# Optimization experiments

Hardware: AMD Instinct MI355X
Metric: run time of the kernel (lower is better)

## Reference

```python
import jax, jax.numpy as jnp
import numpy as np

N, T, D = 50000, 16, 4          # nodes, timesteps, input features
E = 800000                      # edges
H, HID = 4, 32                  # GAT heads, hidden dim (concat=False -> mean over heads)
TH, THID = 4, 64                # temporal heads, temporal hidden (= 2*HID)
HD = THID // TH                 # temporal head dim
NEG_SLOPE = 0.2


def setup_inputs() -> dict:
    key = jax.random.key(0)
    ks = iter(jax.random.split(key, 64))
    nrm = lambda shape, s=0.05: jax.random.normal(next(ks), shape, dtype=jnp.float32) * s
    inp = {}
    inp["x"] = jax.random.normal(next(ks), (N, T, D), dtype=jnp.float32)
    inp["edge_index"] = jax.random.randint(next(ks), (2, E), 0, N)
    inp["edge_weight"] = jax.random.uniform(next(ks), (E,), dtype=jnp.float32)
    # input projection
    inp["in_W"], inp["in_b"] = nrm((D, HID)), nrm((HID,))
    # two GATv2 layers (lin_l, lin_r, lin_edge (no bias), att, out bias)
    for i in range(2):
        inp[f"g{i}_Wl"], inp[f"g{i}_bl"] = nrm((HID, H * HID)), nrm((H * HID,))
        inp[f"g{i}_Wr"], inp[f"g{i}_br"] = nrm((HID, H * HID)), nrm((H * HID,))
        inp[f"g{i}_We"] = nrm((1, H * HID))
        inp[f"g{i}_att"] = nrm((H, HID))
        inp[f"g{i}_bias"] = nrm((HID,))
    # temporal attention block
    inp["Wq"], inp["bq"] = nrm((HID, THID)), nrm((THID,))
    inp["Wk"], inp["bk"] = nrm((HID, THID)), nrm((THID,))
    inp["Wv"], inp["bv"] = nrm((HID, THID)), nrm((THID,))
    inp["Wo"], inp["bo"] = nrm((THID, HID)), nrm((HID,))
    # heads
    inp["fW1"], inp["fb1"] = nrm((HID, 32)), nrm((32,))
    inp["fW2"], inp["fb2"] = nrm((32, 1)), nrm((1,))
    inp["rW1"], inp["rb1"] = nrm((HID, 32)), nrm((32,))
    inp["rW2"], inp["rb2"] = nrm((32, 1)), nrm((1,))
    return inp


def _gatv2(xp, edge_index, edge_attr, Wl, bl, Wr, br, We, att, bias):
    """GATv2Conv, heads=H, concat=False (mean), edge_dim=1, no self loops."""
    src, dst = edge_index[0], edge_index[1]          # message src -> dst
    xl = (xp @ Wl + bl).reshape(N, H, HID)
    xr = (xp @ Wr + br).reshape(N, H, HID)
    ee = (edge_attr @ We).reshape(E, H, HID)
    m = xl[src] + xr[dst] + ee                       # (E,H,C)
    m = jnp.where(m > 0, m, NEG_SLOPE * m)           # leaky_relu
    logits = jnp.einsum('ehc,hc->eh', m, att)        # (E,H)
    mx = jax.ops.segment_max(logits, dst, num_segments=N)
    mx = jnp.where(jnp.isfinite(mx), mx, 0.0)
    a = jnp.exp(logits - mx[dst])
    denom = jax.ops.segment_sum(a, dst, num_segments=N)
    alpha = a / (denom[dst] + 1e-16)                 # segment softmax over dst
    out = jax.ops.segment_sum(alpha[:, :, None] * xl[src], dst, num_segments=N)
    return out.mean(axis=1) + bias                   # (N,HID)


def reference(x, edge_index, edge_weight,
              in_W, in_b,
              g0_Wl, g0_bl, g0_Wr, g0_br, g0_We, g0_att, g0_bias,
              g1_Wl, g1_bl, g1_Wr, g1_br, g1_We, g1_att, g1_bias,
              Wq, bq, Wk, bk, Wv, bv, Wo, bo,
              fW1, fb1, fW2, fb2, rW1, rb1, rW2, rb2):
    edge_attr = edge_weight[:, None]                 # (E,1)
    x_seq = x @ in_W + in_b                          # (N,T,HID)
    x_pool = x_seq.mean(axis=1)                      # (N,HID)
    x_pool = jax.nn.relu(_gatv2(x_pool, edge_index, edge_attr,
                                g0_Wl, g0_bl, g0_Wr, g0_br, g0_We, g0_att, g0_bias))
    x_pool = jax.nn.relu(_gatv2(x_pool, edge_index, edge_attr,
                                g1_Wl, g1_bl, g1_Wr, g1_br, g1_We, g1_att, g1_bias))
    x_seq = x_seq + x_pool[:, None, :]
    node_reps = jnp.transpose(x_seq, (1, 0, 2))      # (T,N,HID)

    def heads(z):                                    # (T,N,THID) -> (N,TH,T,HD)
        return jnp.transpose(z.reshape(T, N, TH, HD), (1, 2, 0, 3))
    Qh = heads(node_reps @ Wq + bq)
    Kh = heads(node_reps @ Wk + bk)
    Vh = heads(node_reps @ Wv + bv)
    scale = HD ** -0.5
    scores = jnp.einsum('bhtd,bhsd->bhts', Qh, Kh) * scale
    w = jax.nn.softmax(scores, axis=-1)
    ctx = jnp.einsum('bhts,bhsd->bhtd', w, Vh)       # (N,TH,T,HD)
    ctx = jnp.transpose(ctx, (2, 0, 1, 3)).reshape(T, N, THID)
    temporal_out = ctx @ Wo + bo                     # (T,N,HID)

    last = temporal_out[-1]                          # (N,HID)
    forecast = jax.nn.relu(jax.nn.relu(last @ fW1 + fb1) @ fW2 + fb2)   # (N,1)
    risk = jax.nn.sigmoid(jax.nn.relu(last @ rW1 + rb1) @ rW2 + rb2)    # (N,1)
    return forecast, risk, temporal_out
```

## Files before the change

kernel.cpp:

```cpp
#include <hip/hip_runtime.h>
#include <hip/hip_bf16.h>

#define NN 50000
#define TT 16
#define DD 4
#define EE 800000
#define HH 4
#define HID 32
#define THID 64
#define HD 16

typedef __attribute__((ext_vector_type(8))) short bf16x8;
typedef __attribute__((ext_vector_type(4))) float f32x4;
typedef __attribute__((ext_vector_type(2))) float f32x2;
typedef __attribute__((ext_vector_type(4))) unsigned u32x4;
typedef __attribute__((ext_vector_type(4))) _Float16 h4;

__device__ __forceinline__ unsigned short f2bf(float f){
    unsigned u = __float_as_uint(f);
    u = u + 0x7fffu + ((u >> 16) & 1u);
    return (unsigned short)(u >> 16);
}
__device__ __forceinline__ unsigned cvtpk(float a, float b){
    unsigned r;
    asm("v_cvt_pk_bf16_f32 %0, %1, %2" : "=v"(r) : "v"(a), "v"(b));
    return r;
}
__device__ __forceinline__ bf16x8 mk8(unsigned a0, unsigned a1, unsigned a2, unsigned a3){
    u32x4 u = {a0, a1, a2, a3};
    return __builtin_bit_cast(bf16x8, u);
}
__device__ __forceinline__ bf16x8 gather8(int d0, int d1, int s0, int s1, bool zero){
    int a0 = __shfl(d0, s0, 64);
    int a1 = __shfl(d1, s0, 64);
    int a2 = __shfl(d0, s1, 64);
    int a3 = __shfl(d1, s1, 64);
    if (zero){ a0 = 0; a1 = 0; a2 = 0; a3 = 0; }
    return mk8((unsigned)a0, (unsigned)a1, (unsigned)a2, (unsigned)a3);
}

__global__ __launch_bounds__(256) void pool_kernel(const float* __restrict__ x,
        const float* __restrict__ in_W, const float* __restrict__ in_b,
        float* __restrict__ xp){
    __shared__ float xs[512];
    __shared__ float xb[8][4];
    int tid = threadIdx.x;
    size_t base = (size_t)blockIdx.x * 512;
    xs[tid]       = x[base + tid];
    xs[tid + 256] = x[base + tid + 256];
    __syncthreads();
    if (tid < 32){
        int nl = tid >> 2, d = tid & 3;
        float s = 0.f;
        #pragma unroll
        for (int t = 0; t < 16; t++) s += xs[nl*64 + t*4 + d];
        xb[nl][d] = s * (1.f/16.f);
    }
    __syncthreads();
    int nl = tid >> 5, c = tid & 31;
    float v = in_b[c];
    #pragma unroll
    for (int d = 0; d < 4; d++) v += xb[nl][d] * in_W[d*32 + c];
    xp[(size_t)(blockIdx.x*8 + nl)*32 + c] = v;
}

__global__ void wfrag_kernel(const float* __restrict__ Wq, const float* __restrict__ Wk,
                             const float* __restrict__ Wv, const float* __restrict__ Wo,
                             unsigned short* __restrict__ frag){
    int fid = blockIdx.x, lane = threadIdx.x;
    const float* W; int b, k0, ncol;
    if (fid < 4)      { W = Wq; b = fid;      k0 = 0;  ncol = 64; }
    else if (fid < 8) { W = Wk; b = fid - 4;  k0 = 0;  ncol = 64; }
    else if (fid < 12){ W = Wv; b = fid - 8;  k0 = 0;  ncol = 64; }
    else { W = Wo; int rb = (fid-12) >> 1, ks = (fid-12) & 1; b = rb; k0 = ks*32; ncol = 32; }
    int col = 16*b + (lane & 15);
    int kk  = k0 + (lane >> 4)*8;
    unsigned short* out = frag + ((size_t)fid*64 + lane)*8;
    #pragma unroll
    for (int j = 0; j < 8; j++) out[j] = f2bf(W[(size_t)(kk + j)*ncol + col]);
}

__global__ void count_kernel(const int* __restrict__ ei, int* __restrict__ counts){
    int e = blockIdx.x*256 + threadIdx.x;
    if (e >= EE) return;
    atomicAdd(&counts[ei[EE + e]], 1);
}

#define SBLK 49

__global__ __launch_bounds__(256) void bsum_kernel(const int* __restrict__ counts,
                                                   int* __restrict__ bsum){
    int b = blockIdx.x, tid = threadIdx.x;
    int base = b*1024 + tid*4;
    int s = 0;
    if (base + 3 < NN){ int4 v = *(const int4*)(counts + base); s = v.x+v.y+v.z+v.w; }
    else { for (int i = 0; i < 4; i++) if (base+i < NN) s += counts[base+i]; }
    #pragma unroll
    for (int off = 1; off < 64; off <<= 1) s += __shfl_xor(s, off, 64);
    __shared__ int wsum[4];
    if ((tid & 63) == 0) wsum[tid >> 6] = s;
    __syncthreads();
    if (tid == 0) bsum[b] = wsum[0] + wsum[1] + wsum[2] + wsum[3];
}

__global__ __launch_bounds__(256) void scan2_kernel(const int* __restrict__ counts,
                                                    const int* __restrict__ bsum,
                                                    int* __restrict__ offs,
                                                    int* __restrict__ nxt){
    int b = blockIdx.x, tid = threadIdx.x;
    __shared__ int lds[256];
    __shared__ int bofs_s;
    if (tid < 64){
        int v = (tid < b) ? bsum[tid] : 0;
        #pragma unroll
        for (int off = 1; off < 64; off <<= 1) v += __shfl_xor(v, off, 64);
        if (tid == 0) bofs_s = v;
    }
    int base = b*1024 + tid*4;
    int c0=0, c1=0, c2=0, c3=0;
    if (base + 3 < NN){ int4 v = *(const int4*)(counts + base); c0=v.x; c1=v.y; c2=v.z; c3=v.w; }
    else {
        if (base   < NN) c0 = counts[base];
        if (base+1 < NN) c1 = counts[base+1];
        if (base+2 < NN) c2 = counts[base+2];
        if (base+3 < NN) c3 = counts[base+3];
    }
    lds[tid] = c0 + c1 + c2 + c3;
    __syncthreads();
    for (int off = 1; off < 256; off <<= 1){
        int v = (tid >= off) ? lds[tid - off] : 0;
        __syncthreads();
        lds[tid] += v;
        __syncthreads();
    }
    int run = bofs_s + ((tid == 0) ? 0 : lds[tid - 1]);
    if (base   < NN){ offs[base]   = run; nxt[base]   = run; } run += c0;
    if (base+1 < NN){ offs[base+1] = run; nxt[base+1] = run; } run += c1;
    if (base+2 < NN){ offs[base+2] = run; nxt[base+2] = run; } run += c2;
    if (base+3 < NN){ offs[base+3] = run; nxt[base+3] = run; }
    if (b == 0 && tid == 0) offs[NN] = EE;
}

__global__ void fill_kernel(const int* __restrict__ ei, const float* __restrict__ ew,
                            int* __restrict__ nxt, int2* __restrict__ esrc){
    int e = blockIdx.x*256 + threadIdx.x;
    if (e >= EE) return;
    int dst = ei[EE + e];
    int pos = atomicAdd(&nxt[dst], 1);
    esrc[pos] = make_int2(ei[e], __float_as_int(ew[e]));
}

#define LNODES 8
__global__ __launch_bounds__(128) void linlr_kernel(const float* __restrict__ xp,
        const float* __restrict__ Wl, const float* __restrict__ bl,
        const float* __restrict__ Wr, const float* __restrict__ br,
        unsigned char* __restrict__ xlf, _Float16* __restrict__ xrh){
    int j = threadIdx.x;
    int n0 = blockIdx.x * LNODES;
    float wl[32], wrr[32];
    #pragma unroll
    for (int k = 0; k < 32; k++){ wl[k] = Wl[k*128 + j]; wrr[k] = Wr[k*128 + j]; }
    float blv = bl[j], brv = br[j];
    __shared__ float xs[LNODES][32];
    int r = j >> 5, c = j & 31;
    #pragma unroll
    for (int q = 0; q < LNODES/4; q++)
        xs[q*4 + r][c] = xp[(size_t)(n0 + q*4 + r)*32 + c];
    __syncthreads();
    #pragma unroll
    for (int m = 0; m < LNODES; m++){
        float al = blv, ar = brv;
        #pragma unroll
        for (int k = 0; k < 32; k++){ float v = xs[m][k]; al += v*wl[k]; ar += v*wrr[k]; }
        unsigned p8 = __builtin_amdgcn_cvt_pk_fp8_f32(al, al, 0u, false);
        xlf[(size_t)(n0+m)*128 + j] = (unsigned char)(p8 & 0xffu);
        xrh[(size_t)(n0+m)*128 + j] = (_Float16)ar;
    }
}

__global__ __launch_bounds__(256) void gat_fused_kernel(
        const int* __restrict__ offs, const int2* __restrict__ esrc,
        const unsigned char* __restrict__ xlf, const _Float16* __restrict__ xrh,
        const float* __restrict__ We, const float* __restrict__ att,
        const float* __restrict__ bias, float* __restrict__ xq){
    int n = blockIdx.x;
    int tid = threadIdx.x;
    int w = tid >> 6, lane = tid & 63;
    int half = lane >> 5, l2 = lane & 31;
    int cb = (l2 >> 3)*32 + (l2 & 7)*4;

    h4 xr4 = __builtin_bit_cast(h4, *(const f32x2*)(xrh + (size_t)n*128 + cb));
    f32x4 wef = {We[cb], We[cb+1], We[cb+2], We[cb+3]};
    h4 We4 = {(_Float16)wef[0], (_Float16)wef[1], (_Float16)wef[2], (_Float16)wef[3]};
    f32x4 atf = {att[cb], att[cb+1], att[cb+2], att[cb+3]};
    h4 at4 = {(_Float16)atf[0], (_Float16)atf[1], (_Float16)atf[2], (_Float16)atf[3]};

    int beg = offs[n], end = offs[n+1];
    float acc0 = 0.f, acc1 = 0.f, acc2 = 0.f, acc3 = 0.f, den = 0.f;
    for (int i = beg + 2*w; i < end; i += 8){
        int e = i + half;
        bool valid = e < end;
        int ec = valid ? e : end - 1;
        int2 r = esrc[ec];
        int src  = r.x;
        float wt = __int_as_float(r.y);
        unsigned u = *(const unsigned*)(xlf + (size_t)src*128 + cb);
        f32x2 lo = __builtin_amdgcn_cvt_pk_f32_fp8(u, false);
        f32x2 hi = __builtin_amdgcn_cvt_pk_f32_fp8(u, true);
        h4 xl4 = {(_Float16)lo[0], (_Float16)lo[1], (_Float16)hi[0], (_Float16)hi[1]};
        h4 m = xl4 + xr4 + We4 * (_Float16)wt;
        h4 rr = __builtin_elementwise_max(m, m * (_Float16)0.2f);
        h4 zp = at4 * rr;
        float z = (float)zp[0] + (float)zp[1] + (float)zp[2] + (float)zp[3];
        z += __shfl_xor(z, 1);
        z += __shfl_xor(z, 2);
        z += __shfl_xor(z, 4);
        float a = valid ? __expf(z) : 0.f;
        den  += a;
        acc0 += a * lo[0];
        acc1 += a * lo[1];
        acc2 += a * hi[0];
        acc3 += a * hi[1];
    }
    __shared__ float lacc[4][64][4];
    __shared__ float lden[4][64];
    lacc[w][lane][0] = acc0;
    lacc[w][lane][1] = acc1;
    lacc[w][lane][2] = acc2;
    lacc[w][lane][3] = acc3;
    lden[w][lane] = den;
    __syncthreads();
    if (tid < 32){
        int j = tid;
        float s = 0.f;
        #pragma unroll
        for (int h = 0; h < 4; h++){
            int lb = h*8 + (j >> 2);
            int sub = j & 3;
            float av = 0.f, dv = 0.f;
            #pragma unroll
            for (int ww = 0; ww < 4; ww++){
                av += lacc[ww][lb][sub] + lacc[ww][lb + 32][sub];
                dv += lden[ww][lb] + lden[ww][lb + 32];
            }
            s += av / (dv + 1e-16f);
        }
        s = s*0.25f + bias[j];
        xq[(size_t)n*32 + j] = fmaxf(s, 0.f);
    }
}

__global__ __launch_bounds__(256) void temporal_kernel(const float* __restrict__ x,
        const float* __restrict__ xpool,
        const float* __restrict__ in_W, const float* __restrict__ in_b,
        const float* __restrict__ bq, const float* __restrict__ bk,
        const float* __restrict__ bv, const float* __restrict__ bo,
        const unsigned short* __restrict__ wfrag,
        const float* __restrict__ fW1, const float* __restrict__ fb1,
        const float* __restrict__ fW2, const float* __restrict__ fb2,
        const float* __restrict__ rW1, const float* __restrict__ rb1,
        const float* __restrict__ rW2, const float* __restrict__ rb2,
        float* __restrict__ out0, float* __restrict__ out1,
        float* __restrict__ out2){
    __shared__ float ctxL[4][64][18];
    int tid = threadIdx.x, w = tid >> 6, lane = tid & 63;
    int n = blockIdx.x*4 + w;
    int t = lane & 15, g = lane >> 4;
    int k0 = g * 8;

    f32x4 xv  = *(const f32x4*)(x + (size_t)n*64 + t*4);
    f32x4 ib0 = *(const f32x4*)(in_b + k0);
    f32x4 ib1 = *(const f32x4*)(in_b + k0 + 4);
    f32x4 xp0 = *(const f32x4*)(xpool + (size_t)n*32 + k0);
    f32x4 xp1 = *(const f32x4*)(xpool + (size_t)n*32 + k0 + 4);
    f32x4 iw0a = *(const f32x4*)(in_W + k0),      iw0b = *(const f32x4*)(in_W + k0 + 4);
    f32x4 iw1a = *(const f32x4*)(in_W + 32 + k0), iw1b = *(const f32x4*)(in_W + 32 + k0 + 4);
    f32x4 iw2a = *(const f32x4*)(in_W + 64 + k0), iw2b = *(const f32x4*)(in_W + 64 + k0 + 4);
    f32x4 iw3a = *(const f32x4*)(in_W + 96 + k0), iw3b = *(const f32x4*)(in_W + 96 + k0 + 4);
    f32x4 sA = ib0 + xp0 + xv[0]*iw0a + xv[1]*iw1a + xv[2]*iw2a + xv[3]*iw3a;
    f32x4 sB = ib1 + xp1 + xv[0]*iw0b + xv[1]*iw1b + xv[2]*iw2b + xv[3]*iw3b;
    bf16x8 sfrag = mk8(cvtpk(sA[0],sA[1]), cvtpk(sA[2],sA[3]), cvtpk(sB[0],sB[1]), cvtpk(sB[2],sB[3]));

    const bf16x8* WF = (const bf16x8*)wfrag;
    f32x4 zero = {0.f, 0.f, 0.f, 0.f};

    int qd0[4], qd1[4], kd0[4], kd1[4], vd0[4], vd1[4];
    #pragma unroll
    for (int b = 0; b < 4; b++){
        bf16x8 wq = WF[(0*4 + b)*64 + lane];
        bf16x8 wk = WF[(1*4 + b)*64 + lane];
        bf16x8 wv = WF[(2*4 + b)*64 + lane];
        f32x4 qc = __builtin_amdgcn_mfma_f32_16x16x32_bf16(wq, sfrag, zero, 0, 0, 0);
        f32x4 kc = __builtin_amdgcn_mfma_f32_16x16x32_bf16(wk, sfrag, zero, 0, 0, 0);
        f32x4 vc = __builtin_amdgcn_mfma_f32_16x16x32_bf16(sfrag, wv, zero, 0, 0, 0);
        f32x4 bq4 = *(const f32x4*)(bq + 16*b + 4*g);
        f32x4 bk4 = *(const f32x4*)(bk + 16*b + 4*g);
        float bvv = bv[16*b + t];
        qc += bq4; kc += bk4;
        vc[0] += bvv; vc[1] += bvv; vc[2] += bvv; vc[3] += bvv;
        qd0[b] = (int)cvtpk(qc[0], qc[1]); qd1[b] = (int)cvtpk(qc[2], qc[3]);
        kd0[b] = (int)cvtpk(kc[0], kc[1]); kd1[b] = (int)cvtpk(kc[2], kc[3]);
        vd0[b] = (int)cvtpk(vc[0], vc[1]); vd1[b] = (int)cvtpk(vc[2], vc[3]);
    }

    int s0l = t + 32*(g & 1);
    int s1l = s0l + 16;
    bool hiz = (g >= 2);
    #pragma unroll
    for (int h = 0; h < 4; h++){
        bf16x8 ka = gather8(kd0[h], kd1[h], s0l, s1l, hiz);
        bf16x8 qb = gather8(qd0[h], qd1[h], s0l, s1l, false);
        f32x4 sc = __builtin_amdgcn_mfma_f32_16x16x32_bf16(ka, qb, zero, 0, 0, 0);
        sc *= 0.25f;
        float m = fmaxf(fmaxf(sc[0], sc[1]), fmaxf(sc[2], sc[3]));
        m = fmaxf(m, __shfl_xor(m, 16, 64));
        m = fmaxf(m, __shfl_xor(m, 32, 64));
        float p0 = __expf(sc[0] - m), p1 = __expf(sc[1] - m);
        float p2 = __expf(sc[2] - m), p3 = __expf(sc[3] - m);
        float sum = p0 + p1 + p2 + p3;
        sum += __shfl_xor(sum, 16, 64);
        sum += __shfl_xor(sum, 32, 64);
        float inv = 1.f / sum;
        int pd0 = (int)cvtpk(p0, p1), pd1 = (int)cvtpk(p2, p3);
        bf16x8 va = gather8(vd0[h], vd1[h], s0l, s1l, hiz);
        bf16x8 pb = gather8(pd0, pd1, s0l, s1l, false);
        f32x4 cx = __builtin_amdgcn_mfma_f32_16x16x32_bf16(va, pb, zero, 0, 0, 0);
        cx *= inv;
        #pragma unroll
        for (int r = 0; r < 4; r++) ctxL[w][h*16 + 4*g + r][t] = cx[r];
    }

    bf16x8 cb[2];
    #pragma unroll
    for (int ks = 0; ks < 2; ks++){
        float c0 = ctxL[w][ks*32 + k0 + 0][t], c1 = ctxL[w][ks*32 + k0 + 1][t];
        float c2 = ctxL[w][ks*32 + k0 + 2][t], c3 = ctxL[w][ks*32 + k0 + 3][t];
        float c4 = ctxL[w][ks*32 + k0 + 4][t], c5 = ctxL[w][ks*32 + k0 + 5][t];
        float c6 = ctxL[w][ks*32 + k0 + 6][t], c7 = ctxL[w][ks*32 + k0 + 7][t];
        cb[ks] = mk8(cvtpk(c0,c1), cvtpk(c2,c3), cvtpk(c4,c5), cvtpk(c6,c7));
    }
    #pragma unroll
    for (int rb = 0; rb < 2; rb++){
        bf16x8 wo0 = WF[(12 + rb*2 + 0)*64 + lane];
        bf16x8 wo1 = WF[(12 + rb*2 + 1)*64 + lane];
        f32x4 oc = __builtin_amdgcn_mfma_f32_16x16x32_bf16(wo0, cb[0], zero, 0, 0, 0);
        oc = __builtin_amdgcn_mfma_f32_16x16x32_bf16(wo1, cb[1], oc, 0, 0, 0);
        f32x4 bo4 = *(const f32x4*)(bo + 16*rb + 4*g);
        oc += bo4;
        #pragma unroll
        for (int r = 0; r < 4; r++) ctxL[w][16*rb + 4*g + r][t] = oc[r];
    }
    float o[8];
    #pragma unroll
    for (int j = 0; j < 8; j++) o[j] = ctxL[w][g*8 + j][t];
    float* outp = out2 + ((size_t)t*NN + n)*32 + g*8;
    *(f32x4*)outp       = (f32x4){o[0], o[1], o[2], o[3]};
    *((f32x4*)outp + 1) = (f32x4){o[4], o[5], o[6], o[7]};

    int cc = lane & 31, path = lane >> 5;
    const float* W1  = path ? rW1 : fW1;
    const float* b1v = path ? rb1 : fb1;
    const float* W2  = path ? rW2 : fW2;
    const float* b2v = path ? rb2 : fb2;
    float h1 = b1v[cc];
    #pragma unroll
    for (int k = 0; k < 32; k++) h1 += ctxL[w][k][15] * W1[k*32 + cc];
    h1 = fmaxf(h1, 0.f);
    float z = h1 * W2[cc];
    #pragma unroll
    for (int off2 = 16; off2 >= 1; off2 >>= 1) z += __shfl_xor(z, off2, 64);
    if (lane == 0)  out0[n] = fmaxf(z + b2v[0], 0.f);
    if (lane == 32) out1[n] = 1.f / (1.f + __expf(-(z + b2v[0])));
}

extern "C" void kernel_launch(void* const* d_in, const int* in_sizes, int n_in,
                              void* d_out, int out_size, void* d_ws, size_t ws_size,
                              hipStream_t stream){
    const float* x    = (const float*)d_in[0];
    const int*   ei   = (const int*)  d_in[1];
    const float* ew   = (const float*)d_in[2];
    const float* in_W = (const float*)d_in[3];
    const float* in_b = (const float*)d_in[4];
    const float* Wq = (const float*)d_in[19];
    const float* bq = (const float*)d_in[20];
    const float* Wk = (const float*)d_in[21];
    const float* bk = (const float*)d_in[22];
    const float* Wv = (const float*)d_in[23];
    const float* bv = (const float*)d_in[24];
    const float* Wo = (const float*)d_in[25];
    const float* bo = (const float*)d_in[26];
    const float* fW1 = (const float*)d_in[27];
    const float* fb1 = (const float*)d_in[28];
    const float* fW2 = (const float*)d_in[29];
    const float* fb2 = (const float*)d_in[30];
    const float* rW1 = (const float*)d_in[31];
    const float* rb1 = (const float*)d_in[32];
    const float* rW2 = (const float*)d_in[33];
    const float* rb2 = (const float*)d_in[34];

    float* out0 = (float*)d_out;
    float* out1 = out0 + NN;
    float* out2 = out0 + 2*NN;

    float* ws = (float*)d_ws;
    size_t off = 0;
    unsigned char* xlf = (unsigned char*)(ws + off); off += (size_t)NN*32;
    _Float16* xrh = (_Float16*)(ws + off); off += (size_t)NN*64;
    float* xpA    = ws + off; off += (size_t)NN*32;
    float* xpB    = ws + off; off += (size_t)NN*32;
    int* counts   = (int*)(ws + off); off += NN;
    int* offs     = (int*)(ws + off); off += NN + 1;
    int* nxt      = (int*)(ws + off); off += NN + 1;
    int* bsum     = (int*)(ws + off); off += SBLK;
    off = (off + 1) & ~(size_t)1;
    int2* esrc    = (int2*)(ws + off); off += (size_t)EE*2;
    off = (off + 3) & ~(size_t)3;
    unsigned short* wfrag = (unsigned short*)(ws + off); off += 16*64*8/2;

    hipMemsetAsync(counts, 0, NN*sizeof(int), stream);
    pool_kernel<<<NN/8, 256, 0, stream>>>(x, in_W, in_b, xpA);
    wfrag_kernel<<<16, 64, 0, stream>>>(Wq, Wk, Wv, Wo, wfrag);
    count_kernel<<<(EE+255)/256, 256, 0, stream>>>(ei, counts);
    bsum_kernel<<<SBLK, 256, 0, stream>>>(counts, bsum);
    scan2_kernel<<<SBLK, 256, 0, stream>>>(counts, bsum, offs, nxt);
    fill_kernel<<<(EE+255)/256, 256, 0, stream>>>(ei, ew, nxt, esrc);

    for (int layer = 0; layer < 2; layer++){
        const float* Wl   = (const float*)d_in[5 + 7*layer];
        const float* bl   = (const float*)d_in[6 + 7*layer];
        const float* Wr   = (const float*)d_in[7 + 7*layer];
        const float* br   = (const float*)d_in[8 + 7*layer];
        const float* We   = (const float*)d_in[9 + 7*layer];
        const float* att  = (const float*)d_in[10 + 7*layer];
        const float* bias = (const float*)d_in[11 + 7*layer];
        const float* xin  = layer ? xpB : xpA;
        float*       xout = layer ? xpA : xpB;
        linlr_kernel<<<NN/LNODES, 128, 0, stream>>>(xin, Wl, bl, Wr, br, xlf, xrh);
        gat_fused_kernel<<<NN, 256, 0, stream>>>(offs, esrc, xlf, xrh, We, att, bias, xout);
    }

    temporal_kernel<<<NN/4, 256, 0, stream>>>(x, xpA, in_W, in_b,
                                              bq, bk, bv, bo, wfrag,
                                              fW1, fb1, fW2, fb2, rW1, rb1, rW2, rb2,
                                              out0, out1, out2);
}
```

Before: 382.1 us.

## Merge prep kernels and widen GAT per-lane channels to eight fp32

Folds the pooling, weight-fragment and edge-count kernels into one launch that dispatches on block index, saving two launch gaps. Rewrites the GAT edge loop so each lane handles 8 channels (16 lanes per edge, 4 edges per wave per step) with fp32 math instead of half-precision 4-wide vectors. This halves the shuffle reduction depth and issues wider 8-byte gathers. The shared-memory final reduction is re-indexed to match. Register use grows, and the switch from fp16 to fp32 arithmetic doubles ALU width per element.

Result: no change. 377.0 us (-1.3%).

```diff
diff --git a/kernel.cpp b/kernel.cpp
--- a/kernel.cpp
+++ b/kernel.cpp
@@ -14,7 +14,7 @@
 typedef __attribute__((ext_vector_type(4))) float f32x4;
 typedef __attribute__((ext_vector_type(2))) float f32x2;
 typedef __attribute__((ext_vector_type(4))) unsigned u32x4;
-typedef __attribute__((ext_vector_type(4))) _Float16 h4;
+typedef __attribute__((ext_vector_type(8))) _Float16 h8;
 
 __device__ __forceinline__ unsigned short f2bf(float f){
     unsigned u = __float_as_uint(f);
@@ -39,51 +39,57 @@
     return mk8((unsigned)a0, (unsigned)a1, (unsigned)a2, (unsigned)a3);
 }
 
-__global__ __launch_bounds__(256) void pool_kernel(const float* __restrict__ x,
+#define POOL_BLKS (NN/8)
+#define WFRAG_BLKS 16
+#define COUNT_BLKS ((EE+255)/256)
+
+__global__ __launch_bounds__(256) void prep_kernel(const float* __restrict__ x,
         const float* __restrict__ in_W, const float* __restrict__ in_b,
-        float* __restrict__ xp){
-    __shared__ float xs[512];
-    __shared__ float xb[8][4];
+        float* __restrict__ xp,
+        const float* __restrict__ Wq, const float* __restrict__ Wk,
+        const float* __restrict__ Wv, const float* __restrict__ Wo,
+        unsigned short* __restrict__ frag,
+        const int* __restrict__ ei, int* __restrict__ counts){
+    int blk = blockIdx.x;
     int tid = threadIdx.x;
-    size_t base = (size_t)blockIdx.x * 512;
-    xs[tid]       = x[base + tid];
-    xs[tid + 256] = x[base + tid + 256];
-    __syncthreads();
-    if (tid < 32){
-        int nl = tid >> 2, d = tid & 3;
-        float s = 0.f;
-        #pragma unroll
-        for (int t = 0; t < 16; t++) s += xs[nl*64 + t*4 + d];
-        xb[nl][d] = s * (1.f/16.f);
-    }
-    __syncthreads();
-    int nl = tid >> 5, c = tid & 31;
-    float v = in_b[c];
-    #pragma unroll
-    for (int d = 0; d < 4; d++) v += xb[nl][d] * in_W[d*32 + c];
-    xp[(size_t)(blockIdx.x*8 + nl)*32 + c] = v;
-}
-
-__global__ void wfrag_kernel(const float* __restrict__ Wq, const float* __restrict__ Wk,
-                             const float* __restrict__ Wv, const float* __restrict__ Wo,
-                             unsigned short* __restrict__ frag){
-    int fid = blockIdx.x, lane = threadIdx.x;
-    const float* W; int b, k0, ncol;
-    if (fid < 4)      { W = Wq; b = fid;      k0 = 0;  ncol = 64; }
-    else if (fid < 8) { W = Wk; b = fid - 4;  k0 = 0;  ncol = 64; }
-    else if (fid < 12){ W = Wv; b = fid - 8;  k0 = 0;  ncol = 64; }
-    else { W = Wo; int rb = (fid-12) >> 1, ks = (fid-12) & 1; b = rb; k0 = ks*32; ncol = 32; }
-    int col = 16*b + (lane & 15);
-    int kk  = k0 + (lane >> 4)*8;
-    unsigned short* out = frag + ((size_t)fid*64 + lane)*8;
-    #pragma unroll
-    for (int j = 0; j < 8; j++) out[j] = f2bf(W[(size_t)(kk + j)*ncol + col]);
-}
-
-__global__ void count_kernel(const int* __restrict__ ei, int* __restrict__ counts){
-    int e = blockIdx.x*256 + threadIdx.x;
-    if (e >= EE) return;
-    atomicAdd(&counts[ei[EE + e]], 1);
+    if (blk < POOL_BLKS){
+        __shared__ float xs[512];
+        __shared__ float xb[8][4];
+        size_t base = (size_t)blk * 512;
+        xs[tid]       = x[base + tid];
+        xs[tid + 256] = x[base + tid + 256];
+        __syncthreads();
+        if (tid < 32){
+            int nl = tid >> 2, d = tid & 3;
+            float s = 0.f;
+            #pragma unroll
+            for (int t = 0; t < 16; t++) s += xs[nl*64 + t*4 + d];
+            xb[nl][d] = s * (1.f/16.f);
+        }
+        __syncthreads();
+        int nl = tid >> 5, c = tid & 31;
+        float v = in_b[c];
+        #pragma unroll
+        for (int d = 0; d < 4; d++) v += xb[nl][d] * in_W[d*32 + c];
+        xp[(size_t)(blk*8 + nl)*32 + c] = v;
+    } else if (blk < POOL_BLKS + WFRAG_BLKS){
+        if (tid < 64){
+            int fid = blk - POOL_BLKS, lane = tid;
+            const float* W; int b, k0, ncol;
+            if (fid < 4)      { W = Wq; b = fid;      k0 = 0;  ncol = 64; }
+            else if (fid < 8) { W = Wk; b = fid - 4;  k0 = 0;  ncol = 64; }
+            else if (fid < 12){ W = Wv; b = fid - 8;  k0 = 0;  ncol = 64; }
+            else { W = Wo; int rb = (fid-12) >> 1, ks = (fid-12) & 1; b = rb; k0 = ks*32; ncol = 32; }
+            int col = 16*b + (lane & 15);
+            int kk  = k0 + (lane >> 4)*8;
+            unsigned short* out = frag + ((size_t)fid*64 + lane)*8;
+            #pragma unroll
+            for (int j = 0; j < 8; j++) out[j] = f2bf(W[(size_t)(kk + j)*ncol + col]);
+        }
+    } else {
+        int e = (blk - POOL_BLKS - WFRAG_BLKS)*256 + tid;
+        if (e < EE) atomicAdd(&counts[ei[EE + e]], 1);
+    }
 }
 
 #define SBLK 49
@@ -186,67 +192,78 @@
     int n = blockIdx.x;
     int tid = threadIdx.x;
     int w = tid >> 6, lane = tid & 63;
-    int half = lane >> 5, l2 = lane & 31;
-    int cb = (l2 >> 3)*32 + (l2 & 7)*4;
-
-    h4 xr4 = __builtin_bit_cast(h4, *(const f32x2*)(xrh + (size_t)n*128 + cb));
-    f32x4 wef = {We[cb], We[cb+1], We[cb+2], We[cb+3]};
-    h4 We4 = {(_Float16)wef[0], (_Float16)wef[1], (_Float16)wef[2], (_Float16)wef[3]};
-    f32x4 atf = {att[cb], att[cb+1], att[cb+2], att[cb+3]};
-    h4 at4 = {(_Float16)atf[0], (_Float16)atf[1], (_Float16)atf[2], (_Float16)atf[3]};
+    int q = lane >> 4, l16 = lane & 15;
+    int cb = l16 * 8;
+
+    float xr[8], Wev[8], atv[8];
+    {
+        f32x4 raw = *(const f32x4*)(xrh + (size_t)n*128 + cb);
+        h8 x8 = __builtin_bit_cast(h8, raw);
+        #pragma unroll
+        for (int j = 0; j < 8; j++) xr[j] = (float)x8[j];
+        f32x4 wa = *(const f32x4*)(We + cb),  wb = *(const f32x4*)(We + cb + 4);
+        f32x4 aa = *(const f32x4*)(att + cb), ab = *(const f32x4*)(att + cb + 4);
+        Wev[0]=wa[0]; Wev[1]=wa[1]; Wev[2]=wa[2]; Wev[3]=wa[3];
+        Wev[4]=wb[0]; Wev[5]=wb[1]; Wev[6]=wb[2]; Wev[7]=wb[3];
+        atv[0]=aa[0]; atv[1]=aa[1]; atv[2]=aa[2]; atv[3]=aa[3];
+        atv[4]=ab[0]; atv[5]=ab[1]; atv[6]=ab[2]; atv[7]=ab[3];
+    }
 
     int beg = offs[n], end = offs[n+1];
-    float acc0 = 0.f, acc1 = 0.f, acc2 = 0.f, acc3 = 0.f, den = 0.f;
-    for (int i = beg + 2*w; i < end; i += 8){
-        int e = i + half;
+    float acc[8] = {0.f,0.f,0.f,0.f,0.f,0.f,0.f,0.f};
+    float den = 0.f;
+    for (int i = beg + 4*w; i < end; i += 16){
+        int e = i + q;
         bool valid = e < end;
         int ec = valid ? e : end - 1;
         int2 r = esrc[ec];
         int src  = r.x;
         float wt = __int_as_float(r.y);
-        unsigned u = *(const unsigned*)(xlf + (size_t)src*128 + cb);
-        f32x2 lo = __builtin_amdgcn_cvt_pk_f32_fp8(u, false);
-        f32x2 hi = __builtin_amdgcn_cvt_pk_f32_fp8(u, true);
-        h4 xl4 = {(_Float16)lo[0], (_Float16)lo[1], (_Float16)hi[0], (_Float16)hi[1]};
-        h4 m = xl4 + xr4 + We4 * (_Float16)wt;
-        h4 rr = __builtin_elementwise_max(m, m * (_Float16)0.2f);
-        h4 zp = at4 * rr;
-        float z = (float)zp[0] + (float)zp[1] + (float)zp[2] + (float)zp[3];
+        uint2 g = *(const uint2*)(xlf + (size_t)src*128 + cb);
+        f32x2 p0 = __builtin_amdgcn_cvt_pk_f32_fp8(g.x, false);
+        f32x2 p1 = __builtin_amdgcn_cvt_pk_f32_fp8(g.x, true);
+        f32x2 p2 = __builtin_amdgcn_cvt_pk_f32_fp8(g.y, false);
+        f32x2 p3 = __builtin_amdgcn_cvt_pk_f32_fp8(g.y, true);
+        float xl[8] = {p0[0],p0[1],p1[0],p1[1],p2[0],p2[1],p3[0],p3[1]};
+        float z = 0.f;
+        #pragma unroll
+        for (int j = 0; j < 8; j++){
+            float m = xl[j] + xr[j] + wt*Wev[j];
+            m = m > 0.f ? m : 0.2f*m;
+            z += m * atv[j];
+        }
         z += __shfl_xor(z, 1);
         z += __shfl_xor(z, 2);
-        z += __shfl_xor(z, 4);
         float a = valid ? __expf(z) : 0.f;
-        den  += a;
-        acc0 += a * lo[0];
-        acc1 += a * lo[1];
-        acc2 += a * hi[0];
-        acc3 += a * hi[1];
-    }
-    __shared__ float lacc[4][64][4];
+        den += a;
+        #pragma unroll
+        for (int j = 0; j < 8; j++) acc[j] += a * xl[j];
+    }
+    __shared__ float lacc[4][8][64];
     __shared__ float lden[4][64];
-    lacc[w][lane][0] = acc0;
-    lacc[w][lane][1] = acc1;
-    lacc[w][lane][2] = acc2;
-    lacc[w][lane][3] = acc3;
+    #pragma unroll
+    for (int j = 0; j < 8; j++) lacc[w][j][lane] = acc[j];
     lden[w][lane] = den;
     __syncthreads();
     if (tid < 32){
-        int j = tid;
         float s = 0.f;
         #pragma unroll
         for (int h = 0; h < 4; h++){
-            int lb = h*8 + (j >> 2);
-            int sub = j & 3;
+            int ach = h*32 + tid;
+            int l = ach >> 3, j = ach & 7;
             float av = 0.f, dv = 0.f;
             #pragma unroll
             for (int ww = 0; ww < 4; ww++){
-                av += lacc[ww][lb][sub] + lacc[ww][lb + 32][sub];
-                dv += lden[ww][lb] + lden[ww][lb + 32];
+                #pragma unroll
+                for (int qq = 0; qq < 4; qq++){
+                    av += lacc[ww][j][qq*16 + l];
+                    dv += lden[ww][qq*16 + h*4];
+                }
             }
             s += av / (dv + 1e-16f);
         }
-        s = s*0.25f + bias[j];
-        xq[(size_t)n*32 + j] = fmaxf(s, 0.f);
+        s = s*0.25f + bias[tid];
+        xq[(size_t)n*32 + tid] = fmaxf(s, 0.f);
     }
 }
 
@@ -418,9 +435,8 @@
     unsigned short* wfrag = (unsigned short*)(ws + off); off += 16*64*8/2;
 
     hipMemsetAsync(counts, 0, NN*sizeof(int), stream);
-    pool_kernel<<<NN/8, 256, 0, stream>>>(x, in_W, in_b, xpA);
-    wfrag_kernel<<<16, 64, 0, stream>>>(Wq, Wk, Wv, Wo, wfrag);
-    count_kernel<<<(EE+255)/256, 256, 0, stream>>>(ei, counts);
+    prep_kernel<<<POOL_BLKS + WFRAG_BLKS + COUNT_BLKS, 256, 0, stream>>>(
+        x, in_W, in_b, xpA, Wq, Wk, Wv, Wo, wfrag, ei, counts);
     bsum_kernel<<<SBLK, 256, 0, stream>>>(counts, bsum);
     scan2_kernel<<<SBLK, 256, 0, stream>>>(counts, bsum, offs, nxt);
     fill_kernel<<<(EE+255)/256, 256, 0, stream>>>(ei, ew, nxt, esrc);
```
